# Optimization experiments

Hardware: AMD Instinct MI355X
Metric: run time of the kernel (lower is better)

The kernel has to match this reference:

```python
import jax, jax.numpy as jnp
import numpy as np

B, S, D, E = 4, 2048, 1024, 8
HD = D // E          # per-expert head dim = 128
ROPE = HD // 2       # rotary dims = 64 (32 complex pairs)


def setup_inputs() -> dict:
    key = jax.random.key(0)
    ks = jax.random.split(key, 5)
    x = jax.random.normal(ks[0], (B, S, D), dtype=jnp.float32)
    Wg = jax.random.normal(ks[1], (D, E), dtype=jnp.float32) * 0.02
    Wqkv = jax.random.normal(ks[2], (E, D, 3 * HD), dtype=jnp.float32) * 0.02
    Wff = jax.random.normal(ks[3], (E, HD, D), dtype=jnp.float32) * 0.02
    b_ff = jnp.zeros((D,), dtype=jnp.float32)
    # precompute_freqs_cis(qk_rope_head_dim=ROPE, seqlen=S), theta=10000
    inv = 1.0 / (10000.0 ** (np.arange(0, ROPE, 2, dtype=np.float32) / ROPE))  # [ROPE//2]
    ang = np.arange(S, dtype=np.float32)[:, None] * inv[None, :]               # [S, ROPE//2]
    cos = jnp.asarray(np.cos(ang), dtype=jnp.float32)
    sin = jnp.asarray(np.sin(ang), dtype=jnp.float32)
    return {"x": x, "Wg": Wg, "Wqkv": Wqkv, "Wff": Wff, "b_ff": b_ff, "cos": cos, "sin": sin}


def _apply_rope(x, cos, sin):
    # x: [B,S,E,HD]; rotate the second half (x_pe), keep first half (x_nope), cat (pe, nope)
    b, s, e, hd = x.shape
    x_nope, x_pe = x[..., : hd // 2], x[..., hd // 2 :]
    xr = x_pe.reshape(b, s, e, hd // 4, 2)
    re, im = xr[..., 0], xr[..., 1]
    c = cos[None, :, None, :]
    sn = sin[None, :, None, :]
    rot = jnp.stack([re * c - im * sn, re * sn + im * c], axis=-1).reshape(b, s, e, hd // 2)
    return jnp.concatenate([rot, x_nope], axis=-1)


def reference(x, Wg, Wqkv, Wff, b_ff, cos, sin):
    b, s, d = x.shape
    e, hd = Wqkv.shape[0], Wqkv.shape[2] // 3
    # RoPE on per-expert chunks
    xh = _apply_rope(x.reshape(b, s, e, hd), cos, sin).reshape(b, s, d)
    # SwitchGate: top-1 routing
    probs = jax.nn.softmax(xh @ Wg, axis=-1)            # [b,s,E]
    expert = jnp.argmax(probs, axis=-1)                 # [b,s]
    gate = jnp.max(probs, axis=-1)                      # [b,s]
    # preprocess: per-expert stable gather of routed tokens (capacity = s, padded+masked)
    is_e = expert[None, :, :] == jnp.arange(e)[:, None, None]        # [E,b,s] bool
    order = jnp.argsort(jnp.where(is_e, 0, 1), axis=-1, stable=True)  # [E,b,s] routed-first
    mask_g = jnp.take_along_axis(is_e, order, axis=-1).astype(xh.dtype)  # [E,b,s]
    x_g = jnp.take_along_axis(xh[None], order[..., None], axis=2)    # [E,b,s,d]
    gate_g = jnp.take_along_axis(gate[None], order, axis=2)          # [E,b,s]
    # expert-grouped column-parallel QKV
    qkv = jnp.einsum("ebsd,edf->ebsf", x_g, Wqkv)                    # [E,b,s,3*hd]
    q, k, v = jnp.split(qkv, 3, axis=-1)                             # [E,b,s,hd]
    # grouped sparse attention within each expert's token set
    dot = jnp.einsum("ebqh,ebkh->ebqk", q, k) / jnp.sqrt(jnp.asarray(hd, xh.dtype))
    dot = dot - 1e6 * (1.0 - mask_g[:, :, None, :])
    attn = jax.nn.softmax(dot, axis=-1)
    ctx = jnp.einsum("ebqk,ebkh->ebqh", attn, v)                     # [E,b,s,hd]
    # row-parallel output projection, gate-weighted
    out = jnp.einsum("ebsh,ehd->ebsd", ctx, Wff) + b_ff
    out = out * (gate_g * mask_g)[..., None]
    # scatter_add combine back to [b,s,d]
    outs = jnp.zeros((b, s, d), dtype=xh.dtype)
    outs = outs.at[jnp.arange(b)[None, :, None], order].add(out)
    return outs
```

## Files before the change

kernel.cpp:

```cpp
#include <hip/hip_runtime.h>
#include <math.h>

#define Bn 4
#define Sn 2048
#define Dn 1024
#define En 8
#define HDn 128
#define NG 32
#define MAXT 160
#define MAXN 1024

typedef __attribute__((ext_vector_type(8))) short bf16x8;
typedef __attribute__((ext_vector_type(4))) float f32x4;
typedef unsigned short u16;

__device__ __forceinline__ unsigned bf16_rn(float x) {
  unsigned u = __float_as_uint(x);
  return (u + 0x7fffu + ((u >> 16) & 1u)) >> 16;
}
__device__ __forceinline__ void bsplit(float x, unsigned& hi, unsigned& lo) {
  hi = bf16_rn(x);
  lo = bf16_rn(x - __uint_as_float(hi << 16));
}
__device__ __forceinline__ void gl16(const void* g, void* l) {
  __builtin_amdgcn_global_load_lds(
      (const __attribute__((address_space(1))) void*)g,
      (__attribute__((address_space(3))) void*)l, 16, 0, 0);
}
#define MFMA16(a, b, c) __builtin_amdgcn_mfma_f32_16x16x32_bf16((a), (b), (c), 0, 0, 0)

__device__ __forceinline__ void prep_body(
    const float* __restrict__ W, u16* __restrict__ hiT, u16* __restrict__ loT,
    int Kdim, int Ndim, int e, int k0, int c0, float (*tile)[65])
{
  int t = threadIdx.x;
  int r = t >> 4, cc = (t & 15) << 2;
  const float* src = W + ((size_t)e * Kdim + k0) * Ndim + c0;
#pragma unroll
  for (int i = 0; i < 4; ++i) {
    float4 v = *(const float4*)(src + (size_t)(r + i * 16) * Ndim + cc);
    tile[r + i * 16][cc + 0] = v.x; tile[r + i * 16][cc + 1] = v.y;
    tile[r + i * 16][cc + 2] = v.z; tile[r + i * 16][cc + 3] = v.w;
  }
  __syncthreads();
#pragma unroll
  for (int i = 0; i < 4; ++i) {
    int oc = (t >> 4) + i * 16;
    int ok = (t & 15) << 2;
    float v0 = tile[ok + 0][oc], v1 = tile[ok + 1][oc];
    float v2 = tile[ok + 2][oc], v3 = tile[ok + 3][oc];
    unsigned h0,l0,h1,l1,h2,l2,h3,l3;
    bsplit(v0,h0,l0); bsplit(v1,h1,l1); bsplit(v2,h2,l2); bsplit(v3,h3,l3);
    size_t o = ((size_t)e * Ndim + c0 + oc) * Kdim + k0 + ok;
    *(ushort4*)(hiT + o) = make_ushort4((u16)h0,(u16)h1,(u16)h2,(u16)h3);
    *(ushort4*)(loT + o) = make_ushort4((u16)l0,(u16)l1,(u16)l2,(u16)l3);
  }
}

__global__ __launch_bounds__(256) void k_prologue(
    const float* __restrict__ x, const float* __restrict__ Wg,
    const float* __restrict__ cosT, const float* __restrict__ sinT,
    const float* __restrict__ Wqkv, const float* __restrict__ Wff,
    u16* __restrict__ xh_hi, u16* __restrict__ xh_lo,
    u16* __restrict__ WqT_hi, u16* __restrict__ WqT_lo,
    u16* __restrict__ WfT_hi, u16* __restrict__ WfT_lo,
    int* __restrict__ expertArr, float* __restrict__ gateArr,
    int* __restrict__ done)
{
  __shared__ float tile[64][65];
  int bid = blockIdx.x;
  if (bid == 0 && threadIdx.x == 0) done[0] = 0;
  if (bid < 2048) {
    int wid = threadIdx.x >> 6, l = threadIdx.x & 63;
    int bs = (bid << 2) + wid;
    int s  = bs & (Sn - 1);
    const float* xrow = x + (size_t)bs * Dn;
    float xa[8], xb[8];
#pragma unroll
    for (int d = 0; d < 8; ++d) {
      xa[d] = xrow[d * 128 + l];
      xb[d] = xrow[d * 128 + 64 + l];
    }
    float ce = cosT[s * 32 + (l >> 1)];
    float sn = sinT[s * 32 + (l >> 1)];
    float ve[8];
#pragma unroll
    for (int d = 0; d < 8; ++d) {
      float self = xb[d];
      float part = __shfl_xor(self, 1, 64);
      ve[d] = (l & 1) ? (part * sn + self * ce) : (self * ce - part * sn);
    }
    size_t obase = (size_t)bs * Dn + l;
#pragma unroll
    for (int d = 0; d < 8; ++d) {
      unsigned h0, l0, h1, l1;
      bsplit(ve[d], h0, l0);
      bsplit(xa[d], h1, l1);
      xh_hi[obase + d * 128]      = (u16)h0;
      xh_lo[obase + d * 128]      = (u16)l0;
      xh_hi[obase + d * 128 + 64] = (u16)h1;
      xh_lo[obase + d * 128 + 64] = (u16)l1;
    }

    float pl[8] = {0.f, 0.f, 0.f, 0.f, 0.f, 0.f, 0.f, 0.f};
#pragma unroll
    for (int d = 0; d < 8; ++d) {
      const float* w0 = Wg + (size_t)(d * 128 + l) * En;
      float4 wA = *(const float4*)w0;
      float4 wB = *(const float4*)(w0 + 4);
      float xv = ve[d];
      pl[0] += xv * wA.x; pl[1] += xv * wA.y; pl[2] += xv * wA.z; pl[3] += xv * wA.w;
      pl[4] += xv * wB.x; pl[5] += xv * wB.y; pl[6] += xv * wB.z; pl[7] += xv * wB.w;
      const float* w1 = Wg + (size_t)(d * 128 + 64 + l) * En;
      float4 wC = *(const float4*)w1;
      float4 wD = *(const float4*)(w1 + 4);
      xv = xa[d];
      pl[0] += xv * wC.x; pl[1] += xv * wC.y; pl[2] += xv * wC.z; pl[3] += xv * wC.w;
      pl[4] += xv * wD.x; pl[5] += xv * wD.y; pl[6] += xv * wD.z; pl[7] += xv * wD.w;
    }
#pragma unroll
    for (int off = 1; off < 64; off <<= 1) {
#pragma unroll
      for (int e = 0; e < 8; ++e) pl[e] += __shfl_xor(pl[e], off, 64);
    }
    float m = pl[0]; int be = 0;
#pragma unroll
    for (int e = 1; e < 8; ++e) if (pl[e] > m) { m = pl[e]; be = e; }
    float ss = 0.f;
#pragma unroll
    for (int e = 0; e < 8; ++e) ss += expf(pl[e] - m);
    if (l == 0) {
      expertArr[bs] = be;
      gateArr[bs] = 1.0f / ss;
    }
  } else if (bid < 2048 + 768) {
    int id = bid - 2048;
    int e = id / 96, r2 = id % 96;
    prep_body(Wqkv, WqT_hi, WqT_lo, Dn, 384, e, (r2 / 6) << 6, (r2 % 6) << 6, tile);
  } else {
    int id = bid - 2816;
    int e = id >> 5, r2 = id & 31;
    prep_body(Wff, WfT_hi, WfT_lo, HDn, Dn, e, (r2 >> 4) << 6, (r2 & 15) << 6, tile);
  }
}

__global__ __launch_bounds__(256) void k_route(
    const int* __restrict__ expertArr, int* __restrict__ idx, int* __restrict__ cnt,
    int* __restrict__ tileg, int* __restrict__ tilem, int* __restrict__ ntile,
    int* __restrict__ done)
{
  int g = blockIdx.x;
  int b = g >> 3, e = g & 7;
  int t = threadIdx.x;
  __shared__ int wtot[4];
  __shared__ int base;
  if (t == 0) base = 0;
  __syncthreads();
  for (int c = 0; c < Sn; c += 256) {
    int s = c + t;
    int pred = (expertArr[b * Sn + s] == e) ? 1 : 0;
    unsigned long long mask = __ballot(pred);
    int ln = t & 63, wv = t >> 6;
    int wpre = __popcll(mask & ((1ull << ln) - 1ull));
    if (ln == 63) wtot[wv] = wpre + pred;
    __syncthreads();
    int woff = 0;
    for (int w = 0; w < wv; ++w) woff += wtot[w];
    int tot = wtot[0] + wtot[1] + wtot[2] + wtot[3];
    if (pred) idx[(g << 11) + base + woff + wpre] = s;
    __syncthreads();
    if (t == 0) base += tot;
    __syncthreads();
  }
  if (t == 0) {
    cnt[g] = base;
    __threadfence();
    if (atomicAdd(done, 1) == NG - 1) {
      int tc = 0;
      for (int gg = 0; gg < NG; ++gg) {
        int nn = __hip_atomic_load(&cnt[gg], __ATOMIC_ACQUIRE, __HIP_MEMORY_SCOPE_AGENT);
        for (int m0 = 0; m0 < nn && tc < MAXT; m0 += 64) { tileg[tc] = gg; tilem[tc] = m0; ++tc; }
      }
      ntile[0] = tc;
    }
  }
}

__global__ __launch_bounds__(256) void k_qkv(
    const u16* __restrict__ xh_hi, const u16* __restrict__ xh_lo,
    const u16* __restrict__ WqT_hi, const u16* __restrict__ WqT_lo,
    const int* __restrict__ idx, const int* __restrict__ cnt,
    u16* __restrict__ qkv_hi, u16* __restrict__ qkv_lo,
    u16* __restrict__ vT_hi, u16* __restrict__ vT_lo)
{
  extern __shared__ unsigned char LDS[];
  int bid = blockIdx.x;
  int r8 = bid & 7, q = bid >> 3;
  int g = r8 + ((q & 3) << 3);
  int slot = q >> 2;
  int m0 = (slot >> 1) << 6;
  int n0 = (slot & 1) * 192;
  int n = cnt[g];
  if (m0 >= n) return;
  int b = g >> 3, e = g & 7;
  const int* idxg = idx + (g << 11);
  int t = threadIdx.x;
  int w = t >> 6, l = t & 63;
  int lc = l & 15, lq = l >> 4;

  int srow = t >> 2;
  int sslot = (t & 3) ^ ((srow >> 1) & 3);
  int rgs = m0 + srow; rgs = rgs < n ? rgs : n - 1;
  size_t aoffR = ((size_t)(b * Sn + idxg[rgs])) * Dn + sslot * 8;
  size_t boffR0 = ((size_t)e * 384 + n0 + srow) * Dn + sslot * 8;
  unsigned dst = (unsigned)t << 4;

  f32x4 acc[4][3];
#pragma unroll
  for (int i = 0; i < 4; ++i)
#pragma unroll
    for (int j = 0; j < 3; ++j) acc[i][j] = (f32x4){0.f, 0.f, 0.f, 0.f};

  unsigned off = (unsigned)((lq ^ ((lc >> 1) & 3)) << 4);

#define STAGE(bb, k0)                                                 \
  do {                                                                \
    gl16(xh_hi + aoffR + (k0), LDS + (bb) + dst);                     \
    gl16(xh_lo + aoffR + (k0), LDS + (bb) + 4096 + dst);              \
    gl16(WqT_hi + boffR0 + (k0), LDS + (bb) + 8192 + dst);            \
    gl16(WqT_hi + boffR0 + (size_t)64 * Dn + (k0), LDS + (bb) + 12288 + dst); \
    gl16(WqT_hi + boffR0 + (size_t)128 * Dn + (k0), LDS + (bb) + 16384 + dst);\
    gl16(WqT_lo + boffR0 + (k0), LDS + (bb) + 20480 + dst);           \
    gl16(WqT_lo + boffR0 + (size_t)64 * Dn + (k0), LDS + (bb) + 24576 + dst); \
    gl16(WqT_lo + boffR0 + (size_t)128 * Dn + (k0), LDS + (bb) + 28672 + dst);\
  } while (0)

  STAGE(0u, 0);
  STAGE(32768u, 32);
  for (int tt = 0; tt < 32; ++tt) {
    unsigned cur = (unsigned)(tt % 3) * 32768u;
    if (tt < 30) {
      STAGE((unsigned)((tt + 2) % 3) * 32768u, (tt + 2) * 32);
      asm volatile("s_waitcnt vmcnt(16)" ::: "memory");
    } else if (tt == 30) {
      asm volatile("s_waitcnt vmcnt(8)" ::: "memory");
    } else {
      asm volatile("s_waitcnt vmcnt(0)" ::: "memory");
    }
    __builtin_amdgcn_s_barrier();
    bf16x8 ah[4], al[4], bh[3], bl[3];
#pragma unroll
    for (int fi = 0; fi < 4; ++fi) {
      unsigned ab = cur + (unsigned)((fi * 16 + lc) * 64) + off;
      ah[fi] = *(const bf16x8*)(LDS + ab);
      al[fi] = *(const bf16x8*)(LDS + ab + 4096);
    }
#pragma unroll
    for (int fj = 0; fj < 3; ++fj) {
      unsigned bb2 = cur + 8192u + (unsigned)((w * 48 + fj * 16 + lc) * 64) + off;
      bh[fj] = *(const bf16x8*)(LDS + bb2);
      bl[fj] = *(const bf16x8*)(LDS + bb2 + 12288);
    }
    __builtin_amdgcn_s_setprio(1);
#pragma unroll
    for (int fi = 0; fi < 4; ++fi)
#pragma unroll
      for (int fj = 0; fj < 3; ++fj) {
        acc[fi][fj] = MFMA16(ah[fi], bh[fj], acc[fi][fj]);
        acc[fi][fj] = MFMA16(al[fi], bh[fj], acc[fi][fj]);
        acc[fi][fj] = MFMA16(ah[fi], bl[fj], acc[fi][fj]);
      }
    __builtin_amdgcn_s_setprio(0);
    asm volatile("s_waitcnt lgkmcnt(0)" ::: "memory");
    __builtin_amdgcn_sched_barrier(0);
    __builtin_amdgcn_s_barrier();
  }
#undef STAGE

#pragma unroll
  for (int fi = 0; fi < 4; ++fi) {
#pragma unroll
    for (int rr = 0; rr < 4; ++rr) {
      int rg = m0 + fi * 16 + lq * 4 + rr;
      if (rg < n) {
        int tok = idxg[rg];
#pragma unroll
        for (int fj = 0; fj < 3; ++fj) {
          int col = n0 + w * 48 + fj * 16 + lc;
          unsigned h, lo2;
          bsplit(acc[fi][fj][rr], h, lo2);
          if (col < 256) {
            size_t o = (size_t)(b * Sn + tok) * 384 + col;
            qkv_hi[o] = (u16)h; qkv_lo[o] = (u16)lo2;
          } else {
            size_t o = ((size_t)g * HDn + (col - 256)) * MAXN + rg;
            vT_hi[o] = (u16)h; vT_lo[o] = (u16)lo2;
          }
        }
      }
    }
  }
}

__global__ __launch_bounds__(256) void k_attn(
    const u16* __restrict__ qkv_hi, const u16* __restrict__ qkv_lo,
    const u16* __restrict__ vT_hi, const u16* __restrict__ vT_lo,
    const int* __restrict__ idx, const int* __restrict__ cnt,
    const int* __restrict__ tileg, const int* __restrict__ tilem,
    const int* __restrict__ ntile,
    u16* __restrict__ ctx_hi, u16* __restrict__ ctx_lo)
{
  extern __shared__ unsigned char LDS[];
  int tid = blockIdx.x;
  if (tid >= ntile[0]) return;
  int g = tileg[tid], m0 = tilem[tid];
  int n = cnt[g];
  int b = g >> 3;
  const int* idxg = idx + (g << 11);
  int t = threadIdx.x, wid = t >> 6, l = t & 63;
  int lc = l & 15, lq = l >> 4;
  const float scale = 0.08838834764831845f;

  int qrg = m0 + wid * 16 + lc; qrg = qrg < n ? qrg : n - 1;
  size_t qoff = (size_t)(b * Sn + idxg[qrg]) * 384 + lq * 8;
  bf16x8 Qhi[4], Qlo[4];
#pragma unroll
  for (int ks = 0; ks < 4; ++ks) {
    Qhi[ks] = *(const bf16x8*)(qkv_hi + qoff + ks * 32);
    Qlo[ks] = *(const bf16x8*)(qkv_lo + qoff + ks * 32);
  }

  f32x4 acc[8];
#pragma unroll
  for (int i = 0; i < 8; ++i) acc[i] = (f32x4){0.f, 0.f, 0.f, 0.f};
  float m_r[4] = {-1e30f, -1e30f, -1e30f, -1e30f};
  float l_r[4] = {0.f, 0.f, 0.f, 0.f};

  size_t vbase = ((size_t)g * HDn + lc) * MAXN + lq * 8;
  unsigned pbase = 65536u + wid * 4096u;

#define STAGEK(bufb, kc)                                                     \
  do {                                                                       \
    unsigned bb = (bufb);                                                    \
    for (int j = 0; j < 4; ++j) {                                            \
      int c = wid * 4 + j;                                                   \
      int row = (kc) + c * 4 + lq;                                           \
      int rg = row < n ? row : n - 1;                                        \
      int srcslot = lc ^ (((c & 1) << 2) | lq);                              \
      size_t soff = (size_t)(b * Sn + idxg[rg]) * 384 + 128 + srcslot * 8;   \
      gl16(qkv_hi + soff, LDS + bb + c * 1024);                              \
      gl16(qkv_lo + soff, LDS + bb + 16384 + c * 1024);                      \
    }                                                                        \
  } while (0)

  int nt = (n + 63) >> 6;
  STAGEK(0, 0);
  asm volatile("s_waitcnt vmcnt(0)" ::: "memory");
  __builtin_amdgcn_s_barrier();

  for (int tt = 0; tt < nt; ++tt) {
    unsigned cur = (tt & 1) ? 32768u : 0u;
    if (tt + 1 < nt) {
      STAGEK(cur ^ 32768u, (tt + 1) * 64);
      asm volatile("s_waitcnt vmcnt(8)" ::: "memory");
    } else {
      asm volatile("s_waitcnt vmcnt(0)" ::: "memory");
    }
    __builtin_amdgcn_s_barrier();
    int kc = tt * 64;

    f32x4 Sf[4];
#pragma unroll
    for (int kf = 0; kf < 4; ++kf) Sf[kf] = (f32x4){0.f, 0.f, 0.f, 0.f};
    __builtin_amdgcn_s_setprio(1);
#pragma unroll
    for (int ks = 0; ks < 4; ++ks) {
#pragma unroll
      for (int kf = 0; kf < 4; ++kf) {
        int row = kf * 16 + lc;
        unsigned byte = cur + row * 256 + ((((ks << 2) | lq) ^ (row & 7)) << 4);
        bf16x8 kh = *(const bf16x8*)(LDS + byte);
        bf16x8 kl = *(const bf16x8*)(LDS + byte + 16384);
        Sf[kf] = MFMA16(Qhi[ks], kh, Sf[kf]);
        Sf[kf] = MFMA16(Qlo[ks], kh, Sf[kf]);
        Sf[kf] = MFMA16(Qhi[ks], kl, Sf[kf]);
      }
    }
    __builtin_amdgcn_s_setprio(0);

    float mloc[4] = {-1e30f, -1e30f, -1e30f, -1e30f};
#pragma unroll
    for (int kf = 0; kf < 4; ++kf) {
#pragma unroll
      for (int r = 0; r < 4; ++r) {
        int key = kc + kf * 16 + lc;
        float s = (key < n) ? Sf[kf][r] * scale : -1e30f;
        Sf[kf][r] = s;
        mloc[r] = fmaxf(mloc[r], s);
      }
    }
#pragma unroll
    for (int off = 1; off < 16; off <<= 1) {
#pragma unroll
      for (int r = 0; r < 4; ++r) mloc[r] = fmaxf(mloc[r], __shfl_xor(mloc[r], off, 64));
    }
    float corr[4], rs[4] = {0.f, 0.f, 0.f, 0.f};
#pragma unroll
    for (int r = 0; r < 4; ++r) {
      float mn = fmaxf(m_r[r], mloc[r]);
      corr[r] = expf(m_r[r] - mn);
      m_r[r] = mn;
    }
#pragma unroll
    for (int kf = 0; kf < 4; ++kf) {
#pragma unroll
      for (int r = 0; r < 4; ++r) {
        float p = expf(Sf[kf][r] - m_r[r]);
        rs[r] += p;
        unsigned ph, plo;
        bsplit(p, ph, plo);
        int prow = (lq << 2) | r;
        int slot = (kf << 1) | (lc >> 3);
        unsigned pb = pbase + prow * 128 + ((slot ^ (prow & 7)) << 4) + ((lc & 7) << 1);
        *(u16*)(LDS + pb) = (u16)ph;
        *(u16*)(LDS + pb + 2048) = (u16)plo;
      }
    }
#pragma unroll
    for (int off = 1; off < 16; off <<= 1) {
#pragma unroll
      for (int r = 0; r < 4; ++r) rs[r] += __shfl_xor(rs[r], off, 64);
    }
#pragma unroll
    for (int r = 0; r < 4; ++r) l_r[r] = l_r[r] * corr[r] + rs[r];
#pragma unroll
    for (int df = 0; df < 8; ++df)
#pragma unroll
      for (int r = 0; r < 4; ++r) acc[df][r] *= corr[r];

#pragma unroll
    for (int ks2 = 0; ks2 < 2; ++ks2) {
      unsigned pr = pbase + lc * 128 + ((((ks2 << 2) | lq) ^ (lc & 7)) << 4);
      bf16x8 pa = *(const bf16x8*)(LDS + pr);
      bf16x8 pl = *(const bf16x8*)(LDS + pr + 2048);
      __builtin_amdgcn_s_setprio(1);
#pragma unroll
      for (int df = 0; df < 8; ++df) {
        size_t vo = vbase + (size_t)(df * 16) * MAXN + kc + ks2 * 32;
        bf16x8 vh = *(const bf16x8*)(vT_hi + vo);
        bf16x8 vl = *(const bf16x8*)(vT_lo + vo);
        acc[df] = MFMA16(pa, vh, acc[df]);
        acc[df] = MFMA16(pl, vh, acc[df]);
        acc[df] = MFMA16(pa, vl, acc[df]);
      }
      __builtin_amdgcn_s_setprio(0);
    }
    asm volatile("s_waitcnt lgkmcnt(0)" ::: "memory");
    __builtin_amdgcn_sched_barrier(0);
    __builtin_amdgcn_s_barrier();
  }
#undef STAGEK

#pragma unroll
  for (int r = 0; r < 4; ++r) {
    int rg = m0 + wid * 16 + (lq << 2) + r;
    if (rg < n) {
      int tok = idxg[rg];
      float inv = 1.0f / l_r[r];
      size_t o = (size_t)(b * Sn + tok) * HDn + lc;
#pragma unroll
      for (int df = 0; df < 8; ++df) {
        unsigned h, lo2;
        bsplit(acc[df][r] * inv, h, lo2);
        ctx_hi[o + df * 16] = (u16)h;
        ctx_lo[o + df * 16] = (u16)lo2;
      }
    }
  }
}

__global__ __launch_bounds__(256) void k_out(
    const u16* __restrict__ ctx_hi, const u16* __restrict__ ctx_lo,
    const u16* __restrict__ WfT_hi, const u16* __restrict__ WfT_lo,
    const float* __restrict__ bff,
    const int* __restrict__ idx, const int* __restrict__ cnt,
    const int* __restrict__ tileg, const int* __restrict__ tilem,
    const int* __restrict__ ntile,
    const float* __restrict__ gateArr,
    float* __restrict__ out)
{
  int tid = blockIdx.x;
  if (tid >= ntile[0]) return;
  int g = tileg[tid], m0 = tilem[tid];
  int n = cnt[g];
  int b = g >> 3, e = g & 7;
  const int* idxg = idx + (g << 11);
  int t = threadIdx.x, wid = t >> 6, l = t & 63;
  int lc = l & 15, lq = l >> 4;
  int n0 = blockIdx.y * 256 + wid * 64;

  f32x4 acc[4][4];
#pragma unroll
  for (int i = 0; i < 4; ++i)
#pragma unroll
    for (int j = 0; j < 4; ++j) acc[i][j] = (f32x4){0.f, 0.f, 0.f, 0.f};

  size_t aoff[4];
#pragma unroll
  for (int fi = 0; fi < 4; ++fi) {
    int rg = m0 + fi * 16 + lc; rg = rg < n ? rg : n - 1;
    aoff[fi] = ((size_t)(b * Sn + idxg[rg])) * HDn + lq * 8;
  }
  size_t boff[4];
#pragma unroll
  for (int fj = 0; fj < 4; ++fj)
    boff[fj] = ((size_t)e * Dn + n0 + fj * 16 + lc) * HDn + lq * 8;

#pragma unroll
  for (int ks = 0; ks < 4; ++ks) {
    int ko = ks * 32;
    bf16x8 ah[4], al[4], bh[4], bl[4];
#pragma unroll
    for (int fi = 0; fi < 4; ++fi) {
      ah[fi] = *(const bf16x8*)(ctx_hi + aoff[fi] + ko);
      al[fi] = *(const bf16x8*)(ctx_lo + aoff[fi] + ko);
    }
#pragma unroll
    for (int fj = 0; fj < 4; ++fj) {
      bh[fj] = *(const bf16x8*)(WfT_hi + boff[fj] + ko);
      bl[fj] = *(const bf16x8*)(WfT_lo + boff[fj] + ko);
    }
#pragma unroll
    for (int fi = 0; fi < 4; ++fi)
#pragma unroll
      for (int fj = 0; fj < 4; ++fj) {
        acc[fi][fj] = MFMA16(ah[fi], bh[fj], acc[fi][fj]);
        acc[fi][fj] = MFMA16(al[fi], bh[fj], acc[fi][fj]);
        acc[fi][fj] = MFMA16(ah[fi], bl[fj], acc[fi][fj]);
      }
  }

  float bv[4];
#pragma unroll
  for (int fj = 0; fj < 4; ++fj) bv[fj] = bff[n0 + fj * 16 + lc];

#pragma unroll
  for (int fi = 0; fi < 4; ++fi) {
#pragma unroll
    for (int rr = 0; rr < 4; ++rr) {
      int rg = m0 + fi * 16 + lq * 4 + rr;
      if (rg < n) {
        int tok = idxg[rg];
        float gt = gateArr[b * Sn + tok];
        float* orow = out + ((size_t)(b * Sn + tok)) * Dn + n0 + lc;
#pragma unroll
        for (int fj = 0; fj < 4; ++fj)
          orow[fj * 16] = (acc[fi][fj][rr] + bv[fj]) * gt;
      }
    }
  }
}

extern "C" void kernel_launch(void* const* d_in, const int* in_sizes, int n_in,
                              void* d_out, int out_size, void* d_ws, size_t ws_size,
                              hipStream_t stream) {
  const float* x    = (const float*)d_in[0];
  const float* Wg   = (const float*)d_in[1];
  const float* Wqkv = (const float*)d_in[2];
  const float* Wff  = (const float*)d_in[3];
  const float* bff  = (const float*)d_in[4];
  const float* cosT = (const float*)d_in[5];
  const float* sinT = (const float*)d_in[6];
  float* out = (float*)d_out;

  size_t off = 0;
  auto carve = [&](size_t bytes) -> void* {
    void* p = (char*)d_ws + off;
    off += (bytes + 255) & ~(size_t)255;
    return p;
  };
  u16* xh_hi  = (u16*)carve((size_t)Bn * Sn * Dn * 2);
  u16* xh_lo  = (u16*)carve((size_t)Bn * Sn * Dn * 2);
  u16* WqT_hi = (u16*)carve((size_t)En * 384 * Dn * 2);
  u16* WqT_lo = (u16*)carve((size_t)En * 384 * Dn * 2);
  u16* WfT_hi = (u16*)carve((size_t)En * Dn * HDn * 2);
  u16* WfT_lo = (u16*)carve((size_t)En * Dn * HDn * 2);
  u16* qkv_hi = (u16*)carve((size_t)Bn * Sn * 384 * 2);
  u16* qkv_lo = (u16*)carve((size_t)Bn * Sn * 384 * 2);
  u16* vT_hi  = (u16*)carve((size_t)NG * HDn * MAXN * 2);
  u16* vT_lo  = (u16*)carve((size_t)NG * HDn * MAXN * 2);
  u16* ctx_hi = (u16*)carve((size_t)Bn * Sn * HDn * 2);
  u16* ctx_lo = (u16*)carve((size_t)Bn * Sn * HDn * 2);
  float* gateArr = (float*)carve((size_t)Bn * Sn * sizeof(float));
  int*   expertA = (int*)carve((size_t)Bn * Sn * sizeof(int));
  int*   idx     = (int*)carve((size_t)NG * Sn * sizeof(int));
  int*   cnt     = (int*)carve((size_t)NG * sizeof(int));
  int*   tileg   = (int*)carve((size_t)MAXT * sizeof(int));
  int*   tilem   = (int*)carve((size_t)MAXT * sizeof(int));
  int*   ntile   = (int*)carve(256);
  int*   done    = (int*)carve(256);
  (void)ws_size; (void)in_sizes; (void)n_in; (void)out_size;

  hipFuncSetAttribute((const void*)k_qkv, hipFuncAttributeMaxDynamicSharedMemorySize, 98304);
  hipFuncSetAttribute((const void*)k_attn, hipFuncAttributeMaxDynamicSharedMemorySize, 81920);

  k_prologue<<<dim3(3072), dim3(256), 0, stream>>>(x, Wg, cosT, sinT, Wqkv, Wff,
      xh_hi, xh_lo, WqT_hi, WqT_lo, WfT_hi, WfT_lo, expertA, gateArr, done);
  k_route<<<dim3(NG), dim3(256), 0, stream>>>(expertA, idx, cnt, tileg, tilem, ntile, done);
  k_qkv<<<dim3(384), dim3(256), 98304, stream>>>(xh_hi, xh_lo, WqT_hi, WqT_lo, idx, cnt, qkv_hi, qkv_lo, vT_hi, vT_lo);
  k_attn<<<dim3(MAXT), dim3(256), 81920, stream>>>(qkv_hi, qkv_lo, vT_hi, vT_lo, idx, cnt, tileg, tilem, ntile, ctx_hi, ctx_lo);
  k_out<<<dim3(MAXT, 4), dim3(256), 0, stream>>>(ctx_hi, ctx_lo, WfT_hi, WfT_lo, bff, idx, cnt, tileg, tilem, ntile, gateArr, out);
}
```

Before: 181.6 us.

## Pre-gather routed tokens into contiguous per-group buffers and double-buffer QKV staging

Adds a k_gather kernel that copies each group's routed rows of the hi/lo split activations into a contiguous per-group buffer (capacity 384 rows). QKV, attention and output kernels then address q/k and ctx through this grouped layout instead of indirecting through idx. The QKV loop also drops from triple to double buffering, cutting dynamic LDS from 96KB to 64KB, which may allow more resident blocks per CU. The cost is an extra launch plus a full copy pass over the gathered activations, and less prefetch depth in the QKV main loop.

```diff
diff --git a/kernel.cpp b/kernel.cpp
--- a/kernel.cpp
+++ b/kernel.cpp
@@ -8,6 +8,7 @@
 #define HDn 128
 #define NG 32
 #define MAXT 160
+#define GN 384
 #define MAXN 1024
 
 typedef __attribute__((ext_vector_type(8))) short bf16x8;
@@ -186,11 +187,33 @@
   }
 }
 
+__global__ __launch_bounds__(256) void k_gather(
+    const u16* __restrict__ xh_hi, const u16* __restrict__ xh_lo,
+    const int* __restrict__ idx, const int* __restrict__ cnt,
+    u16* __restrict__ xg_hi, u16* __restrict__ xg_lo)
+{
+  int g = blockIdx.x;
+  int n = cnt[g];
+  int t = threadIdx.x;
+  int r = (blockIdx.y << 4) + (t >> 4);
+  if (r >= n) return;
+  int tok = idx[(g << 11) + r];
+  size_t s = ((size_t)((g >> 3) * Sn + tok)) << 10;
+  size_t d = ((size_t)(g * GN + r)) << 10;
+  int c0 = (t & 15) << 6;
+#pragma unroll
+  for (int j = 0; j < 8; ++j) {
+    int c = c0 + j * 8;
+    *(uint4*)(xg_hi + d + c) = *(const uint4*)(xh_hi + s + c);
+    *(uint4*)(xg_lo + d + c) = *(const uint4*)(xh_lo + s + c);
+  }
+}
+
 __global__ __launch_bounds__(256) void k_qkv(
-    const u16* __restrict__ xh_hi, const u16* __restrict__ xh_lo,
+    const u16* __restrict__ xg_hi, const u16* __restrict__ xg_lo,
     const u16* __restrict__ WqT_hi, const u16* __restrict__ WqT_lo,
-    const int* __restrict__ idx, const int* __restrict__ cnt,
-    u16* __restrict__ qkv_hi, u16* __restrict__ qkv_lo,
+    const int* __restrict__ cnt,
+    u16* __restrict__ qkvg_hi, u16* __restrict__ qkvg_lo,
     u16* __restrict__ vT_hi, u16* __restrict__ vT_lo)
 {
   extern __shared__ unsigned char LDS[];
@@ -202,16 +225,14 @@
   int n0 = (slot & 1) * 192;
   int n = cnt[g];
   if (m0 >= n) return;
-  int b = g >> 3, e = g & 7;
-  const int* idxg = idx + (g << 11);
+  int e = g & 7;
   int t = threadIdx.x;
   int w = t >> 6, l = t & 63;
   int lc = l & 15, lq = l >> 4;
 
   int srow = t >> 2;
   int sslot = (t & 3) ^ ((srow >> 1) & 3);
-  int rgs = m0 + srow; rgs = rgs < n ? rgs : n - 1;
-  size_t aoffR = ((size_t)(b * Sn + idxg[rgs])) * Dn + sslot * 8;
+  size_t aoffR = ((size_t)(g * GN + m0 + srow)) * Dn + sslot * 8;
   size_t boffR0 = ((size_t)e * 384 + n0 + srow) * Dn + sslot * 8;
   unsigned dst = (unsigned)t << 4;
 
@@ -225,8 +246,8 @@
 
 #define STAGE(bb, k0)                                                 \
   do {                                                                \
-    gl16(xh_hi + aoffR + (k0), LDS + (bb) + dst);                     \
-    gl16(xh_lo + aoffR + (k0), LDS + (bb) + 4096 + dst);              \
+    gl16(xg_hi + aoffR + (k0), LDS + (bb) + dst);                     \
+    gl16(xg_lo + aoffR + (k0), LDS + (bb) + 4096 + dst);              \
     gl16(WqT_hi + boffR0 + (k0), LDS + (bb) + 8192 + dst);            \
     gl16(WqT_hi + boffR0 + (size_t)64 * Dn + (k0), LDS + (bb) + 12288 + dst); \
     gl16(WqT_hi + boffR0 + (size_t)128 * Dn + (k0), LDS + (bb) + 16384 + dst);\
@@ -235,14 +256,13 @@
     gl16(WqT_lo + boffR0 + (size_t)128 * Dn + (k0), LDS + (bb) + 28672 + dst);\
   } while (0)
 
-  STAGE(0u, 0);
-  STAGE(32768u, 32);
+  STAGE(0, 0);
+  asm volatile("s_waitcnt vmcnt(0)" ::: "memory");
+  __builtin_amdgcn_s_barrier();
   for (int tt = 0; tt < 32; ++tt) {
-    unsigned cur = (unsigned)(tt % 3) * 32768u;
-    if (tt < 30) {
-      STAGE((unsigned)((tt + 2) % 3) * 32768u, (tt + 2) * 32);
-      asm volatile("s_waitcnt vmcnt(16)" ::: "memory");
-    } else if (tt == 30) {
+    unsigned cur = (tt & 1) ? 32768u : 0u;
+    if (tt < 31) {
+      STAGE(cur ^ 32768u, (tt + 1) * 32);
       asm volatile("s_waitcnt vmcnt(8)" ::: "memory");
     } else {
       asm volatile("s_waitcnt vmcnt(0)" ::: "memory");
@@ -283,15 +303,14 @@
     for (int rr = 0; rr < 4; ++rr) {
       int rg = m0 + fi * 16 + lq * 4 + rr;
       if (rg < n) {
-        int tok = idxg[rg];
 #pragma unroll
         for (int fj = 0; fj < 3; ++fj) {
           int col = n0 + w * 48 + fj * 16 + lc;
           unsigned h, lo2;
           bsplit(acc[fi][fj][rr], h, lo2);
           if (col < 256) {
-            size_t o = (size_t)(b * Sn + tok) * 384 + col;
-            qkv_hi[o] = (u16)h; qkv_lo[o] = (u16)lo2;
+            size_t o = (size_t)(g * GN + rg) * 256 + col;
+            qkvg_hi[o] = (u16)h; qkvg_lo[o] = (u16)lo2;
           } else {
             size_t o = ((size_t)g * HDn + (col - 256)) * MAXN + rg;
             vT_hi[o] = (u16)h; vT_lo[o] = (u16)lo2;
@@ -303,31 +322,29 @@
 }
 
 __global__ __launch_bounds__(256) void k_attn(
-    const u16* __restrict__ qkv_hi, const u16* __restrict__ qkv_lo,
+    const u16* __restrict__ qkvg_hi, const u16* __restrict__ qkvg_lo,
     const u16* __restrict__ vT_hi, const u16* __restrict__ vT_lo,
-    const int* __restrict__ idx, const int* __restrict__ cnt,
+    const int* __restrict__ cnt,
     const int* __restrict__ tileg, const int* __restrict__ tilem,
     const int* __restrict__ ntile,
-    u16* __restrict__ ctx_hi, u16* __restrict__ ctx_lo)
+    u16* __restrict__ ctxg_hi, u16* __restrict__ ctxg_lo)
 {
   extern __shared__ unsigned char LDS[];
   int tid = blockIdx.x;
   if (tid >= ntile[0]) return;
   int g = tileg[tid], m0 = tilem[tid];
   int n = cnt[g];
-  int b = g >> 3;
-  const int* idxg = idx + (g << 11);
   int t = threadIdx.x, wid = t >> 6, l = t & 63;
   int lc = l & 15, lq = l >> 4;
   const float scale = 0.08838834764831845f;
 
   int qrg = m0 + wid * 16 + lc; qrg = qrg < n ? qrg : n - 1;
-  size_t qoff = (size_t)(b * Sn + idxg[qrg]) * 384 + lq * 8;
+  size_t qoff = (size_t)(g * GN + qrg) * 256 + lq * 8;
   bf16x8 Qhi[4], Qlo[4];
 #pragma unroll
   for (int ks = 0; ks < 4; ++ks) {
-    Qhi[ks] = *(const bf16x8*)(qkv_hi + qoff + ks * 32);
-    Qlo[ks] = *(const bf16x8*)(qkv_lo + qoff + ks * 32);
+    Qhi[ks] = *(const bf16x8*)(qkvg_hi + qoff + ks * 32);
+    Qlo[ks] = *(const bf16x8*)(qkvg_lo + qoff + ks * 32);
   }
 
   f32x4 acc[8];
@@ -347,9 +364,9 @@
       int row = (kc) + c * 4 + lq;                                           \
       int rg = row < n ? row : n - 1;                                        \
       int srcslot = lc ^ (((c & 1) << 2) | lq);                              \
-      size_t soff = (size_t)(b * Sn + idxg[rg]) * 384 + 128 + srcslot * 8;   \
-      gl16(qkv_hi + soff, LDS + bb + c * 1024);                              \
-      gl16(qkv_lo + soff, LDS + bb + 16384 + c * 1024);                      \
+      size_t soff = (size_t)(g * GN + rg) * 256 + 128 + srcslot * 8;         \
+      gl16(qkvg_hi + soff, LDS + bb + c * 1024);                             \
+      gl16(qkvg_lo + soff, LDS + bb + 16384 + c * 1024);                     \
     }                                                                        \
   } while (0)
 
@@ -420,8 +437,8 @@
         unsigned ph, plo;
         bsplit(p, ph, plo);
         int prow = (lq << 2) | r;
-        int slot = (kf << 1) | (lc >> 3);
-        unsigned pb = pbase + prow * 128 + ((slot ^ (prow & 7)) << 4) + ((lc & 7) << 1);
+        int slotp = (kf << 1) | (lc >> 3);
+        unsigned pb = pbase + prow * 128 + ((slotp ^ (prow & 7)) << 4) + ((lc & 7) << 1);
         *(u16*)(LDS + pb) = (u16)ph;
         *(u16*)(LDS + pb + 2048) = (u16)plo;
       }
@@ -465,22 +482,21 @@
   for (int r = 0; r < 4; ++r) {
     int rg = m0 + wid * 16 + (lq << 2) + r;
     if (rg < n) {
-      int tok = idxg[rg];
       float inv = 1.0f / l_r[r];
-      size_t o = (size_t)(b * Sn + tok) * HDn + lc;
+      size_t o = (size_t)(g * GN + rg) * HDn + lc;
 #pragma unroll
       for (int df = 0; df < 8; ++df) {
         unsigned h, lo2;
         bsplit(acc[df][r] * inv, h, lo2);
-        ctx_hi[o + df * 16] = (u16)h;
-        ctx_lo[o + df * 16] = (u16)lo2;
+        ctxg_hi[o + df * 16] = (u16)h;
+        ctxg_lo[o + df * 16] = (u16)lo2;
       }
     }
   }
 }
 
 __global__ __launch_bounds__(256) void k_out(
-    const u16* __restrict__ ctx_hi, const u16* __restrict__ ctx_lo,
+    const u16* __restrict__ ctxg_hi, const u16* __restrict__ ctxg_lo,
     const u16* __restrict__ WfT_hi, const u16* __restrict__ WfT_lo,
     const float* __restrict__ bff,
     const int* __restrict__ idx, const int* __restrict__ cnt,
@@ -509,7 +525,7 @@
 #pragma unroll
   for (int fi = 0; fi < 4; ++fi) {
     int rg = m0 + fi * 16 + lc; rg = rg < n ? rg : n - 1;
-    aoff[fi] = ((size_t)(b * Sn + idxg[rg])) * HDn + lq * 8;
+    aoff[fi] = ((size_t)(g * GN + rg)) * HDn + lq * 8;
   }
   size_t boff[4];
 #pragma unroll
@@ -522,8 +538,8 @@
     bf16x8 ah[4], al[4], bh[4], bl[4];
 #pragma unroll
     for (int fi = 0; fi < 4; ++fi) {
-      ah[fi] = *(const bf16x8*)(ctx_hi + aoff[fi] + ko);
-      al[fi] = *(const bf16x8*)(ctx_lo + aoff[fi] + ko);
+      ah[fi] = *(const bf16x8*)(ctxg_hi + aoff[fi] + ko);
+      al[fi] = *(const bf16x8*)(ctxg_lo + aoff[fi] + ko);
     }
 #pragma unroll
     for (int fj = 0; fj < 4; ++fj) {
@@ -579,18 +595,20 @@
     off += (bytes + 255) & ~(size_t)255;
     return p;
   };
-  u16* xh_hi  = (u16*)carve((size_t)Bn * Sn * Dn * 2);
-  u16* xh_lo  = (u16*)carve((size_t)Bn * Sn * Dn * 2);
-  u16* WqT_hi = (u16*)carve((size_t)En * 384 * Dn * 2);
-  u16* WqT_lo = (u16*)carve((size_t)En * 384 * Dn * 2);
-  u16* WfT_hi = (u16*)carve((size_t)En * Dn * HDn * 2);
-  u16* WfT_lo = (u16*)carve((size_t)En * Dn * HDn * 2);
-  u16* qkv_hi = (u16*)carve((size_t)Bn * Sn * 384 * 2);
-  u16* qkv_lo = (u16*)carve((size_t)Bn * Sn * 384 * 2);
-  u16* vT_hi  = (u16*)carve((size_t)NG * HDn * MAXN * 2);
-  u16* vT_lo  = (u16*)carve((size_t)NG * HDn * MAXN * 2);
-  u16* ctx_hi = (u16*)carve((size_t)Bn * Sn * HDn * 2);
-  u16* ctx_lo = (u16*)carve((size_t)Bn * Sn * HDn * 2);
+  u16* xh_hi   = (u16*)carve((size_t)Bn * Sn * Dn * 2);
+  u16* xh_lo   = (u16*)carve((size_t)Bn * Sn * Dn * 2);
+  u16* xg_hi   = (u16*)carve((size_t)NG * GN * Dn * 2);
+  u16* xg_lo   = (u16*)carve((size_t)NG * GN * Dn * 2);
+  u16* WqT_hi  = (u16*)carve((size_t)En * 384 * Dn * 2);
+  u16* WqT_lo  = (u16*)carve((size_t)En * 384 * Dn * 2);
+  u16* WfT_hi  = (u16*)carve((size_t)En * Dn * HDn * 2);
+  u16* WfT_lo  = (u16*)carve((size_t)En * Dn * HDn * 2);
+  u16* qkvg_hi = (u16*)carve((size_t)NG * GN * 256 * 2);
+  u16* qkvg_lo = (u16*)carve((size_t)NG * GN * 256 * 2);
+  u16* vT_hi   = (u16*)carve((size_t)NG * HDn * MAXN * 2);
+  u16* vT_lo   = (u16*)carve((size_t)NG * HDn * MAXN * 2);
+  u16* ctxg_hi = (u16*)carve((size_t)NG * GN * HDn * 2);
+  u16* ctxg_lo = (u16*)carve((size_t)NG * GN * HDn * 2);
   float* gateArr = (float*)carve((size_t)Bn * Sn * sizeof(float));
   int*   expertA = (int*)carve((size_t)Bn * Sn * sizeof(int));
   int*   idx     = (int*)carve((size_t)NG * Sn * sizeof(int));
@@ -601,13 +619,17 @@
   int*   done    = (int*)carve(256);
   (void)ws_size; (void)in_sizes; (void)n_in; (void)out_size;
 
-  hipFuncSetAttribute((const void*)k_qkv, hipFuncAttributeMaxDynamicSharedMemorySize, 98304);
+  hipFuncSetAttribute((const void*)k_qkv, hipFuncAttributeMaxDynamicSharedMemorySize, 65536);
   hipFuncSetAttribute((const void*)k_attn, hipFuncAttributeMaxDynamicSharedMemorySize, 81920);
 
   k_prologue<<<dim3(3072), dim3(256), 0, stream>>>(x, Wg, cosT, sinT, Wqkv, Wff,
       xh_hi, xh_lo, WqT_hi, WqT_lo, WfT_hi, WfT_lo, expertA, gateArr, done);
   k_route<<<dim3(NG), dim3(256), 0, stream>>>(expertA, idx, cnt, tileg, tilem, ntile, done);
-  k_qkv<<<dim3(384), dim3(256), 98304, stream>>>(xh_hi, xh_lo, WqT_hi, WqT_lo, idx, cnt, qkv_hi, qkv_lo, vT_hi, vT_lo);
-  k_attn<<<dim3(MAXT), dim3(256), 81920, stream>>>(qkv_hi, qkv_lo, vT_hi, vT_lo, idx, cnt, tileg, tilem, ntile, ctx_hi, ctx_lo);
-  k_out<<<dim3(MAXT, 4), dim3(256), 0, stream>>>(ctx_hi, ctx_lo, WfT_hi, WfT_lo, bff, idx, cnt, tileg, tilem, ntile, gateArr, out);
-}
+  k_gather<<<dim3(NG, GN / 16), dim3(256), 0, stream>>>(xh_hi, xh_lo, idx, cnt, xg_hi, xg_lo);
+  k_qkv<<<dim3(384), dim3(256), 65536, stream>>>(xg_hi, xg_lo, WqT_hi, WqT_lo, cnt,
+      qkvg_hi, qkvg_lo, vT_hi, vT_lo);
+  k_attn<<<dim3(MAXT), dim3(256), 81920, stream>>>(qkvg_hi, qkvg_lo, vT_hi, vT_lo, cnt,
+      tileg, tilem, ntile, ctxg_hi, ctxg_lo);
+  k_out<<<dim3(MAXT, 4), dim3(256), 0, stream>>>(ctxg_hi, ctxg_lo, WfT_hi, WfT_lo, bff,
+      idx, cnt, tileg, tilem, ntile, gateArr, out);
+}
```

New measurement: 191.6 us. 1.06x slower.
